# Kernel tuning notes

Hardware: AMD Instinct MI355X
Metric: run time of the kernel (lower is better)

## Reference

```python
import jax, jax.numpy as jnp
import numpy as np

B, S, D = 2, 2048, 2048
H = 16
HD = D // H  # 128
ROPE_THETA = 10000.0


def _rotate_half(x):
    # interleaved rotate: [-x2_0, x1_0, -x2_1, x1_1, ...]
    x1 = x[..., ::2]
    x2 = x[..., 1::2]
    return jnp.stack((-x2, x1), axis=-1).reshape(x.shape)


def _rope_cos_sin(seq_len, head_dim, dtype):
    inv_freq = 1.0 / (ROPE_THETA ** (jnp.arange(0, head_dim, 2, dtype=jnp.float32) / head_dim))
    pos = jnp.arange(seq_len, dtype=jnp.float32)
    freqs = pos[:, None] * inv_freq[None, :]          # [S, HD/2]
    angles = jnp.concatenate((freqs, freqs), axis=-1)  # [S, HD]  (matches torch.cat((freqs, freqs), -1))
    return jnp.cos(angles).astype(dtype), jnp.sin(angles).astype(dtype)


def setup_inputs() -> dict:
    key = jax.random.key(0)
    ks = jax.random.split(key, 5)
    scale = 1.0 / np.sqrt(D)
    return {
        "x": jax.random.normal(ks[0], (B, S, D), dtype=jnp.float32),
        "Wq": jax.random.normal(ks[1], (D, D), dtype=jnp.float32) * scale,
        "Wk": jax.random.normal(ks[2], (D, D), dtype=jnp.float32) * scale,
        "Wv": jax.random.normal(ks[3], (D, D), dtype=jnp.float32) * scale,
        "Wo": jax.random.normal(ks[4], (D, D), dtype=jnp.float32) * scale,
    }


def reference(x, Wq, Wk, Wv, Wo):
    b, s, d = x.shape
    # separate Q/K/V projections (no bias), reshape to [B, H, S, HD]
    def proj(W):
        return jnp.einsum('bsd,de->bse', x, W).reshape(b, s, H, HD).transpose(0, 2, 1, 3)
    q, k, v = proj(Wq), proj(Wk), proj(Wv)

    cos, sin = _rope_cos_sin(s, HD, q.dtype)  # [S, HD]
    cos = cos[None, None, :, :]
    sin = sin[None, None, :, :]
    q = q * cos + _rotate_half(q) * sin
    k = k * cos + _rotate_half(k) * sin

    # causal scaled dot-product attention
    scores = jnp.einsum('bhqd,bhkd->bhqk', q, k) / jnp.sqrt(jnp.asarray(HD, q.dtype))
    causal = jnp.tril(jnp.ones((s, s), dtype=bool))
    scores = jnp.where(causal[None, None, :, :], scores, jnp.asarray(-jnp.inf, scores.dtype))
    attn = jax.nn.softmax(scores, axis=-1)
    out = jnp.einsum('bhqk,bhkd->bhqd', attn, v)

    out = out.transpose(0, 2, 1, 3).reshape(b, s, d)
    return jnp.einsum('bsd,de->bse', out, Wo)
```

## Files before the change

kernel.cpp:

```cpp
#include <hip/hip_runtime.h>
#include <hip/hip_bf16.h>
#include <math.h>

typedef unsigned short u16;
typedef unsigned int u32;

#define Bz 2
#define Sz 2048
#define Dz 2048
#define Hz 16
#define HDz 128
#define Mz 4096

typedef __bf16 bf16x8 __attribute__((ext_vector_type(8)));
typedef float f32x4 __attribute__((ext_vector_type(4)));

__device__ __forceinline__ float bf2f(u16 h) {
    union { u32 u; float f; } x; x.u = ((u32)h) << 16; return x.f;
}
__device__ __forceinline__ u16 f2bf(float f) {
    union { float f; u32 u; } x; x.f = f;
    u32 u = x.u;
    return (u16)((u + 0x7FFFu + ((u >> 16) & 1u)) >> 16);
}
__device__ __forceinline__ u32 pack_bf16_trunc(float lo, float hi) {
    union { float f; u32 u; } a, b; a.f = lo; b.f = hi;
    return (a.u >> 16) | (b.u & 0xFFFF0000u);
}
__device__ __forceinline__ u32 pack_bf16_rn(float lo, float hi) {
    return (u32)f2bf(lo) | ((u32)f2bf(hi) << 16);
}
__device__ __forceinline__ float fexp2(float x) {
#if __has_builtin(__builtin_amdgcn_exp2f)
    return __builtin_amdgcn_exp2f(x);
#else
    return exp2f(x);
#endif
}
__device__ __forceinline__ void sincos_rev(float tr, float* sn, float* cn) {
#if __has_builtin(__builtin_amdgcn_fractf) && __has_builtin(__builtin_amdgcn_sinf) && __has_builtin(__builtin_amdgcn_cosf)
    float fu = __builtin_amdgcn_fractf(tr);
    *sn = __builtin_amdgcn_sinf(fu);
    *cn = __builtin_amdgcn_cosf(fu);
#else
    sincosf(tr * 6.283185307179586f, sn, cn);
#endif
}
__device__ __forceinline__ void gl_lds16(const void* g, void* l) {
    __builtin_amdgcn_global_load_lds(
        (const __attribute__((address_space(1))) void*)g,
        (__attribute__((address_space(3))) void*)l, 16, 0, 0);
}

__global__ void prep(const float* __restrict__ x, const float* __restrict__ W0,
                     const float* __restrict__ W1, const float* __restrict__ W2,
                     const float* __restrict__ W3, u16* __restrict__ Wt,
                     u16* __restrict__ xb) {
    const int z = blockIdx.z;
    if (z >= 4) {
        size_t bid = (size_t)(blockIdx.y * 32 + blockIdx.x) + (size_t)(z - 4) * 1024;
        size_t i = bid * 256 + threadIdx.x;
        float4 a = ((const float4*)x)[2 * i];
        float4 b = ((const float4*)x)[2 * i + 1];
        u16 r[8] = {f2bf(a.x), f2bf(a.y), f2bf(a.z), f2bf(a.w),
                    f2bf(b.x), f2bf(b.y), f2bf(b.z), f2bf(b.w)};
        *(uint4*)(xb + 8 * i) = *(const uint4*)r;
        return;
    }
    __shared__ u16 t[64][65];
    const float* src = (z == 0) ? W0 : (z == 1) ? W1 : (z == 2) ? W2 : W3;
    u16* dst = Wt + (size_t)z * (Dz * Dz);
    int x0 = blockIdx.x * 64, y0 = blockIdx.y * 64;
    {
        int c4 = (threadIdx.x & 15) * 4, r0 = (threadIdx.x >> 4) * 4;
#pragma unroll
        for (int i = 0; i < 4; i++) {
            int r = r0 + i;
            float4 v = *(const float4*)&src[(size_t)(y0 + r) * Dz + x0 + c4];
            t[r][c4 + 0] = f2bf(v.x); t[r][c4 + 1] = f2bf(v.y);
            t[r][c4 + 2] = f2bf(v.z); t[r][c4 + 3] = f2bf(v.w);
        }
    }
    __syncthreads();
    {
        int ce = (threadIdx.x & 31) * 2, r0 = (threadIdx.x >> 5) * 8;
#pragma unroll
        for (int j = 0; j < 8; j++) {
            int r = r0 + j;
            u32 w = (u32)t[ce][r] | ((u32)t[ce + 1][r] << 16);
            *(u32*)&dst[(size_t)(x0 + r) * Dz + y0 + ce] = w;
        }
    }
}

template <int MODE>
__global__ void gemm_bt(const u16* __restrict__ A, const u16* __restrict__ BtBase,
                        void* __restrict__ CBase) {
    const int z = blockIdx.z;
    const u16* Bt = BtBase + (size_t)z * (Dz * Dz);
    const int tid = threadIdx.x, lane = tid & 63, wave = tid >> 6;
    const int ln = lane & 15, qd = lane >> 4;
    const int lid = blockIdx.y * 16 + blockIdx.x;
    const int wid = (lid & 7) * 64 + (lid >> 3);
    const int m0 = (wid >> 4) * 128, n0 = (wid & 15) * 128;

    __shared__ __align__(16) u16 As[128][64];
    __shared__ __align__(16) u16 Bs[128][64];

    f32x4 acc[4][4];
#pragma unroll
    for (int i = 0; i < 4; i++)
#pragma unroll
        for (int j = 0; j < 4; j++) acc[i][j] = (f32x4){0.f, 0.f, 0.f, 0.f};

    const int wm = (wave >> 1) * 64, wn = (wave & 1) * 64;
    const int lr8 = lane >> 3;
    const int bgo = (((lane & 7) ^ lr8) * 8);
    const int x7 = ln & 7;

    for (int k0 = 0; k0 < Dz; k0 += 64) {
        const u16* ga = A  + (size_t)(m0 + wave * 32 + lr8) * Dz + k0 + bgo;
        const u16* gb = Bt + (size_t)(n0 + wave * 32 + lr8) * Dz + k0 + bgo;
#pragma unroll
        for (int i = 0; i < 4; i++) {
            gl_lds16(ga + (size_t)(8 * i) * Dz, &As[wave * 32 + 8 * i][0]);
            gl_lds16(gb + (size_t)(8 * i) * Dz, &Bs[wave * 32 + 8 * i][0]);
        }
        __syncthreads();
#pragma unroll
        for (int kc = 0; kc < 2; kc++) {
            bf16x8 af[4], bff[4];
            const int cs = ((4 * kc + qd) ^ x7) * 8;
#pragma unroll
            for (int i = 0; i < 4; i++) {
                af[i]  = *(const bf16x8*)&As[wm + i * 16 + ln][cs];
                bff[i] = *(const bf16x8*)&Bs[wn + i * 16 + ln][cs];
            }
#pragma unroll
            for (int i = 0; i < 4; i++)
#pragma unroll
                for (int j = 0; j < 4; j++)
                    acc[i][j] = __builtin_amdgcn_mfma_f32_16x16x32_bf16(
                        af[i], bff[j], acc[i][j], 0, 0, 0);
        }
        __syncthreads();
    }

#pragma unroll
    for (int i = 0; i < 4; i++) {
#pragma unroll
        for (int j = 0; j < 4; j++) {
#pragma unroll
            for (int r = 0; r < 4; r++) {
                int row = m0 + wm + i * 16 + qd * 4 + r;
                int col = n0 + wn + j * 16 + ln;
                if (MODE == 0) {
                    ((float*)CBase)[(size_t)row * Dz + col] = acc[i][j][r];
                } else {
                    u16* C = (u16*)CBase + (size_t)z * ((size_t)Mz * Dz);
                    float v = acc[i][j][r];
                    int bb = row >> 11, ss = row & 2047;
                    int hh = col >> 7, hd = col & 127;
                    if (z == 2) {
                        C[((size_t)(bb * Hz + hh) * HDz + hd) * Sz + ss] = f2bf(v);
                    } else {
                        float partner = __shfl_xor(v, 1);
                        const float LG = 0.20762050593046017f;
                        const float L2PI = 2.6514961294723187f;
                        float fr = fexp2(-LG * (float)(hd & 63) - L2PI);
                        float sn, cn;
                        sincos_rev((float)ss * fr, &sn, &cn);
                        float rot = (hd & 1) ? partner : -partner;
                        float y = v * cn + rot * sn;
                        if (z == 0) y *= 0.12751771218027603f;
                        C[((size_t)(bb * Hz + hh) * Sz + ss) * HDz + hd] = f2bf(y);
                    }
                }
            }
        }
    }
}

__global__ __launch_bounds__(256, 4)
void flash_attn(const u16* __restrict__ Q, const u16* __restrict__ Kk,
                const u16* __restrict__ Vt, u16* __restrict__ O) {
    const int tid = threadIdx.x, lane = tid & 63, wave = tid >> 6;
    const int ln = lane & 15, qd = lane >> 4;
    const int bh = blockIdx.x & 31;
    const int g = blockIdx.x >> 5;
    const int gm = g & 7, gj = g >> 3;
    const int qt = (gj == 0) ? gm : (gj == 1) ? 31 - gm
                 : (gj == 2) ? 8 + gm : 23 - gm;
    const int b = bh >> 4, h = bh & 15;
    const int q0 = qt * 64;
    const u16* Qh = Q  + (size_t)bh * Sz * HDz;
    const u16* Kh = Kk + (size_t)bh * Sz * HDz;
    const u16* Vh = Vt + (size_t)bh * HDz * Sz;

    __shared__ __align__(16) u16 Ks[64][128];
    __shared__ __align__(16) u16 Vs[128][64];

    const int qabs = q0 + wave * 16 + ln;
    bf16x8 qf[4];
#pragma unroll
    for (int kc = 0; kc < 4; kc++) {
        uint4 t = *(const uint4*)(Qh + (size_t)qabs * HDz + kc * 32 + qd * 8);
        qf[kc] = *(const bf16x8*)&t;
    }

    float m_run = -INFINITY;
    float l_run = 0.f;
    f32x4 oa[8];
#pragma unroll
    for (int n = 0; n < 8; n++) oa[n] = (f32x4){0.f, 0.f, 0.f, 0.f};

    const int x7 = ln & 7;
    const int l4 = lane >> 4, c16 = lane & 15;
    const int lr8 = lane >> 3;
    const int bgv = ((lane & 7) ^ lr8) * 8;

    for (int k0 = 0; k0 <= q0; k0 += 64) {
        {
#pragma unroll
            for (int i = 0; i < 4; i++) {
                int rw = 4 * (i & 1) + l4;
                const u16* gk = Kh + (size_t)(k0 + 16 * wave + 4 * i + l4) * HDz
                                   + ((c16 ^ rw) * 8);
                gl_lds16(gk, &Ks[16 * wave + 4 * i][0]);
            }
            const u16* gv = Vh + (size_t)(32 * wave + lr8) * Sz + k0 + bgv;
#pragma unroll
            for (int i = 0; i < 4; i++)
                gl_lds16(gv + (size_t)(8 * i) * Sz, &Vs[32 * wave + 8 * i][0]);
        }
        __syncthreads();

        f32x4 sc4[4];
#pragma unroll
        for (int mt = 0; mt < 4; mt++) sc4[mt] = (f32x4){0.f, 0.f, 0.f, 0.f};
#pragma unroll
        for (int kc = 0; kc < 4; kc++) {
            const int cs = ((4 * kc + qd) ^ x7) * 8;
#pragma unroll
            for (int mt = 0; mt < 4; mt++) {
                bf16x8 kf = *(const bf16x8*)&Ks[mt * 16 + ln][cs];
                sc4[mt] = __builtin_amdgcn_mfma_f32_16x16x32_bf16(kf, qf[kc], sc4[mt], 0, 0, 0);
            }
        }
        if (k0 == q0) {
#pragma unroll
            for (int mt = 0; mt < 4; mt++)
#pragma unroll
                for (int r = 0; r < 4; r++)
                    if (mt * 16 + qd * 4 + r > 16 * wave + ln) sc4[mt][r] = -3e38f;
        }

        float rm = -3e38f;
#pragma unroll
        for (int mt = 0; mt < 4; mt++) {
            rm = fmaxf(rm, fmaxf(fmaxf(sc4[mt][0], sc4[mt][1]),
                                 fmaxf(sc4[mt][2], sc4[mt][3])));
        }
        rm = fmaxf(rm, __shfl_xor(rm, 16));
        rm = fmaxf(rm, __shfl_xor(rm, 32));
        if (__ballot(rm > m_run + 8.f) != 0ULL) {
            float mn = fmaxf(m_run, rm);
            float al = fexp2(m_run - mn);
            m_run = mn;
            l_run *= al;
#pragma unroll
            for (int n = 0; n < 8; n++)
#pragma unroll
                for (int r = 0; r < 4; r++) oa[n][r] *= al;
        }

        u32 pku[8];
        float ls = 0.f;
#pragma unroll
        for (int mt = 0; mt < 4; mt++) {
#pragma unroll
            for (int t = 0; t < 2; t++) {
                u32 w = pack_bf16_trunc(fexp2(sc4[mt][2 * t] - m_run),
                                        fexp2(sc4[mt][2 * t + 1] - m_run));
                pku[mt * 2 + t] = w;
                union { u32 u; float f; } t0, t1;
                t0.u = w << 16; t1.u = w & 0xFFFF0000u;
                ls += t0.f + t1.f;
            }
        }
        ls += __shfl_xor(ls, 16);
        ls += __shfl_xor(ls, 32);
        l_run += ls;

#pragma unroll
        for (int kc = 0; kc < 2; kc++) {
            union { u32 w[4]; bf16x8 v; } pb;
#pragma unroll
            for (int s = 0; s < 4; s++) {
                int srcl = ((2 * (qd & 1) + (s >> 1)) << 4) | ln;
                u32 a0 = (u32)__shfl((int)pku[4 * kc + (s & 1)], srcl);
                u32 a1 = (u32)__shfl((int)pku[4 * kc + 2 + (s & 1)], srcl);
                pb.w[s] = (qd & 2) ? a1 : a0;
            }
            const int cs = ((4 * kc + qd) ^ x7) * 8;
#pragma unroll
            for (int mt = 0; mt < 8; mt++) {
                bf16x8 vf = *(const bf16x8*)&Vs[mt * 16 + ln][cs];
                oa[mt] = __builtin_amdgcn_mfma_f32_16x16x32_bf16(vf, pb.v, oa[mt], 0, 0, 0);
            }
        }
        __syncthreads();
    }

    float linv = 1.0f / l_run;
    u16* op = O + ((size_t)b * Sz + qabs) * Dz + h * HDz;
#pragma unroll
    for (int mt = 0; mt < 8; mt++) {
        u32 w0 = pack_bf16_rn(oa[mt][0] * linv, oa[mt][1] * linv);
        u32 w1 = pack_bf16_rn(oa[mt][2] * linv, oa[mt][3] * linv);
        uint2 ww; ww.x = w0; ww.y = w1;
        *(uint2*)(op + mt * 16 + qd * 4) = ww;
    }
}

extern "C" void kernel_launch(void* const* d_in, const int* in_sizes, int n_in,
                              void* d_out, int out_size, void* d_ws, size_t ws_size,
                              hipStream_t stream) {
    const float* x  = (const float*)d_in[0];
    const float* Wq = (const float*)d_in[1];
    const float* Wk = (const float*)d_in[2];
    const float* Wv = (const float*)d_in[3];
    const float* Wo = (const float*)d_in[4];
    u16* ws  = (u16*)d_ws;

    u16* wt = ws;
    u16* q  = ws + 16777216;
    u16* kk = q + 8388608;
    u16* v  = kk + 8388608;
    u16* xb = v + 8388608;
    u16* o  = xb;

    prep<<<dim3(32, 32, 8), 256, 0, stream>>>(x, Wq, Wk, Wv, Wo, wt, xb);
    gemm_bt<1><<<dim3(16, 32, 3), 256, 0, stream>>>(xb, wt, q);
    flash_attn<<<dim3(1024), 256, 0, stream>>>(q, kk, v, o);
    gemm_bt<0><<<dim3(16, 32, 1), 256, 0, stream>>>(o, wt + 3 * 4194304, (float*)d_out);
}
```

Before: 340.0 us.

## Load K and V fragments directly from global memory, dropping LDS staging

Removes the shared-memory K/V tiles and the direct-to-LDS loads, so each wave reads its K and V MFMA fragments straight from global memory (through the caches). This drops both block barriers per key tile and the LDS footprint, which may allow more resident blocks. In exchange, each of the four waves now fetches the same K/V data separately, so global/L2 traffic per block roughly quadruples. The loads are also no longer issued ahead of the compute, which exposes memory latency.

```diff
diff --git a/kernel.cpp b/kernel.cpp
--- a/kernel.cpp
+++ b/kernel.cpp
@@ -197,9 +197,6 @@
     const u16* Kh = Kk + (size_t)bh * Sz * HDz;
     const u16* Vh = Vt + (size_t)bh * HDz * Sz;
 
-    __shared__ __align__(16) u16 Ks[64][128];
-    __shared__ __align__(16) u16 Vs[128][64];
-
     const int qabs = q0 + wave * 16 + ln;
     bf16x8 qf[4];
 #pragma unroll
@@ -214,36 +211,17 @@
 #pragma unroll
     for (int n = 0; n < 8; n++) oa[n] = (f32x4){0.f, 0.f, 0.f, 0.f};
 
-    const int x7 = ln & 7;
-    const int l4 = lane >> 4, c16 = lane & 15;
-    const int lr8 = lane >> 3;
-    const int bgv = ((lane & 7) ^ lr8) * 8;
-
     for (int k0 = 0; k0 <= q0; k0 += 64) {
-        {
-#pragma unroll
-            for (int i = 0; i < 4; i++) {
-                int rw = 4 * (i & 1) + l4;
-                const u16* gk = Kh + (size_t)(k0 + 16 * wave + 4 * i + l4) * HDz
-                                   + ((c16 ^ rw) * 8);
-                gl_lds16(gk, &Ks[16 * wave + 4 * i][0]);
-            }
-            const u16* gv = Vh + (size_t)(32 * wave + lr8) * Sz + k0 + bgv;
-#pragma unroll
-            for (int i = 0; i < 4; i++)
-                gl_lds16(gv + (size_t)(8 * i) * Sz, &Vs[32 * wave + 8 * i][0]);
-        }
-        __syncthreads();
-
         f32x4 sc4[4];
 #pragma unroll
         for (int mt = 0; mt < 4; mt++) sc4[mt] = (f32x4){0.f, 0.f, 0.f, 0.f};
 #pragma unroll
         for (int kc = 0; kc < 4; kc++) {
-            const int cs = ((4 * kc + qd) ^ x7) * 8;
+            const int kcol = (4 * kc + qd) * 8;
 #pragma unroll
             for (int mt = 0; mt < 4; mt++) {
-                bf16x8 kf = *(const bf16x8*)&Ks[mt * 16 + ln][cs];
+                uint4 t = *(const uint4*)(Kh + (size_t)(k0 + mt * 16 + ln) * HDz + kcol);
+                bf16x8 kf = *(const bf16x8*)&t;
                 sc4[mt] = __builtin_amdgcn_mfma_f32_16x16x32_bf16(kf, qf[kc], sc4[mt], 0, 0, 0);
             }
         }
@@ -302,14 +280,14 @@
                 u32 a1 = (u32)__shfl((int)pku[4 * kc + 2 + (s & 1)], srcl);
                 pb.w[s] = (qd & 2) ? a1 : a0;
             }
-            const int cs = ((4 * kc + qd) ^ x7) * 8;
+            const int vcol = k0 + (4 * kc + qd) * 8;
 #pragma unroll
             for (int mt = 0; mt < 8; mt++) {
-                bf16x8 vf = *(const bf16x8*)&Vs[mt * 16 + ln][cs];
+                uint4 t = *(const uint4*)(Vh + (size_t)(mt * 16 + ln) * Sz + vcol);
+                bf16x8 vf = *(const bf16x8*)&t;
                 oa[mt] = __builtin_amdgcn_mfma_f32_16x16x32_bf16(vf, pb.v, oa[mt], 0, 0, 0);
             }
         }
-        __syncthreads();
     }
 
     float linv = 1.0f / l_run;
```

After: 541.1 us. +59.2%, slower.
